# Performance work log

Hardware: AMD Instinct MI355X
Metric: run time of the kernel (lower is better)

The kernel has to match this reference:

```python
import jax, jax.numpy as jnp
import numpy as np

WINDOW_SIZES = (4, 8, 16, 32)


def setup_inputs() -> dict:
    key = jax.random.key(0)
    k1, k2 = jax.random.split(key)
    B, L, D = 128, 1024, 128
    sequence_emb = jax.random.normal(k1, (B, L, D), dtype=jnp.float32)
    mask = jax.random.randint(k2, (B, L), 0, 2, dtype=jnp.int32)
    return {"sequence_emb": sequence_emb, "mask": mask}


def reference(sequence_emb, mask):
    # sequence_emb: (B, L, D); mask: (B, L) int 0/1
    B, L, D = sequence_emb.shape
    m = mask.astype(sequence_emb.dtype)
    masked = sequence_emb * m[..., None]  # (B, L, D)
    # prefix sums with leading zero so window sum = cs[i+w] - cs[i]
    zero_v = jnp.zeros((B, 1, D), dtype=sequence_emb.dtype)
    cs = jnp.concatenate([zero_v, jnp.cumsum(masked, axis=1)], axis=1)  # (B, L+1, D)
    zero_m = jnp.zeros((B, 1), dtype=sequence_emb.dtype)
    cm = jnp.concatenate([zero_m, jnp.cumsum(m, axis=1)], axis=1)  # (B, L+1)
    outs = []
    for w in WINDOW_SIZES:
        if L < w:
            continue
        win_sum = cs[:, w:, :] - cs[:, :-w, :]          # (B, L-w+1, D)
        win_len = jnp.clip(cm[:, w:] - cm[:, :-w], 1.0)  # (B, L-w+1)
        outs.append(win_sum / win_len[..., None])
    return jnp.concatenate(outs, axis=1)  # (B, sum(L-w+1), D)
```

## Files before the change

kernel.cpp:

```cpp
#include <hip/hip_runtime.h>


namespace {
constexpr int kB    = 128;
constexpr int kL    = 1024;
constexpr int kD    = 128;
constexpr int kD4   = kD / 4;
constexpr int TILE  = 64;
constexpr int HALO  = 32;
constexpr int ROWS  = TILE + HALO;
constexpr int ROUT  = 4040;
constexpr int OFF4  = 0;
constexpr int OFF8  = 1021;
constexpr int OFF16 = 2038;
constexpr int OFF32 = 3047;
}

__device__ __forceinline__ void acc4(float4& a, const float4& x) {
    a.x += x.x; a.y += x.y; a.z += x.z; a.w += x.w;
}
__device__ __forceinline__ void slide4(float4& a, const float4& xin, const float4& xout) {
    a.x += xin.x - xout.x; a.y += xin.y - xout.y;
    a.z += xin.z - xout.z; a.w += xin.w - xout.w;
}
__device__ __forceinline__ float4 scale4(const float4& v, float s) {
    return make_float4(v.x * s, v.y * s, v.z * s, v.w * s);
}

__global__ __launch_bounds__(256)
void msse_kernel(const float* __restrict__ emb,
                 const int*   __restrict__ mask,
                 float*       __restrict__ out) {
    __shared__ float4 s_data[ROWS * kD4];
    __shared__ float  s_mask[ROWS];
    __shared__ float  s_inv[4][TILE];

    const int b  = blockIdx.y;
    const int i0 = blockIdx.x * TILE;
    const int t  = threadIdx.x;

    const float4* gsrc = reinterpret_cast<const float4*>(emb) + (size_t)b * kL * kD4;
    #pragma unroll
    for (int k = 0; k < (ROWS * kD4) / 256; ++k) {
        const int f    = t + k * 256;
        const int row  = f >> 5;
        const int grow = i0 + row;
        float4 v = make_float4(0.f, 0.f, 0.f, 0.f);
        float  m = 0.f;
        if (grow < kL) {
            m = (float)mask[b * kL + grow];
            v = gsrc[grow * kD4 + (f & 31)];
            v.x *= m; v.y *= m; v.z *= m; v.w *= m;
        }
        s_data[f] = v;
        if ((f & 31) == 0) s_mask[row] = m;
    }
    __syncthreads();

    if (t < TILE) {
        float c = 0.f, c4 = 0.f, c8 = 0.f, c16 = 0.f;
        #pragma unroll
        for (int j = 0; j < 32; ++j) {
            c += s_mask[t + j];
            if (j == 3)  c4  = c;
            if (j == 7)  c8  = c;
            if (j == 15) c16 = c;
        }
        s_inv[0][t] = 1.f / fmaxf(c4,  1.f);
        s_inv[1][t] = 1.f / fmaxf(c8,  1.f);
        s_inv[2][t] = 1.f / fmaxf(c16, 1.f);
        s_inv[3][t] = 1.f / fmaxf(c,   1.f);
    }
    __syncthreads();

    const int lane  = t & 31;
    const int strip = t >> 5;
    const int base  = strip * 8;

    const float4* col = s_data + lane;

    float4 s4, s8, s16, s32;
    {
        float4 a  = make_float4(0.f, 0.f, 0.f, 0.f);
        float4 t4 = a, t8 = a, t16 = a;
        #pragma unroll
        for (int j = 0; j < 32; ++j) {
            acc4(a, col[(base + j) * kD4]);
            if (j == 3)  t4  = a;
            if (j == 7)  t8  = a;
            if (j == 15) t16 = a;
        }
        s4 = t4; s8 = t8; s16 = t16; s32 = a;
    }

    float4* outb = reinterpret_cast<float4*>(out) + (size_t)b * ROUT * kD4 + lane;

    #pragma unroll
    for (int p = 0; p < 8; ++p) {
        const int il = base + p;
        const int i  = i0 + il;

        if (i <= kL - 4)  outb[(OFF4  + i) * kD4] = scale4(s4,  s_inv[0][il]);
        if (i <= kL - 8)  outb[(OFF8  + i) * kD4] = scale4(s8,  s_inv[1][il]);
        if (i <= kL - 16) outb[(OFF16 + i) * kD4] = scale4(s16, s_inv[2][il]);
        if (i <= kL - 32) outb[(OFF32 + i) * kD4] = scale4(s32, s_inv[3][il]);

        const float4 x0 = col[(il)      * kD4];
        const float4 xa = col[(il + 4)  * kD4];
        const float4 xb = col[(il + 8)  * kD4];
        const float4 xc = col[(il + 16) * kD4];
        const float4 xd = col[(il + 32) * kD4];
        slide4(s4,  xa, x0);
        slide4(s8,  xb, x0);
        slide4(s16, xc, x0);
        slide4(s32, xd, x0);
    }
}

extern "C" void kernel_launch(void* const* d_in, const int* in_sizes, int n_in,
                              void* d_out, int out_size, void* d_ws, size_t ws_size,
                              hipStream_t stream) {
    const float* emb  = (const float*)d_in[0];
    const int*   mask = (const int*)d_in[1];
    float*       out  = (float*)d_out;

    dim3 grid((kL + TILE - 1) / TILE, kB);
    dim3 block(256);
    msse_kernel<<<grid, block, 0, stream>>>(emb, mask, out);
}
```

Baseline: 315.8 us.

## Drop shared-memory staging, stream rows per wave with nontemporal stores and precomputed inverses

Replaces the LDS-tiled kernel with a per-wave strip design: each 64-lane wave owns 32 output positions of one batch row and reads embedding rows straight from global memory as float2, with each row re-read several times through the caches. Inverse window lengths move into a separate pre-kernel that writes float4 inverses to the workspace. Output stores become nontemporal. The aim is to remove LDS traffic and barriers and to raise occupancy. The cost is redundant global and L2 reads, a second kernel launch, and narrower 8-byte accesses.

```diff
diff --git a/kernel.cpp b/kernel.cpp
--- a/kernel.cpp
+++ b/kernel.cpp
@@ -2,90 +2,79 @@
 
 
 namespace {
-constexpr int kB    = 128;
-constexpr int kL    = 1024;
-constexpr int kD    = 128;
-constexpr int kD4   = kD / 4;
-constexpr int TILE  = 64;
-constexpr int HALO  = 32;
-constexpr int ROWS  = TILE + HALO;
-constexpr int ROUT  = 4040;
+constexpr int kB   = 128;
+constexpr int kL   = 1024;
+constexpr int kD   = 128;
+constexpr int kD2  = kD / 2;
+constexpr int ROUT = 4040;
 constexpr int OFF4  = 0;
 constexpr int OFF8  = 1021;
 constexpr int OFF16 = 2038;
 constexpr int OFF32 = 3047;
+constexpr int P    = 32;
+constexpr int STRIPS = kB * (kL / P);
 }
 
-__device__ __forceinline__ void acc4(float4& a, const float4& x) {
-    a.x += x.x; a.y += x.y; a.z += x.z; a.w += x.w;
+typedef float v2f __attribute__((ext_vector_type(2)));
+
+__device__ __forceinline__ void nt_store2(v2f* p, v2f v) {
+    __builtin_nontemporal_store(v, p);
 }
-__device__ __forceinline__ void slide4(float4& a, const float4& xin, const float4& xout) {
-    a.x += xin.x - xout.x; a.y += xin.y - xout.y;
-    a.z += xin.z - xout.z; a.w += xin.w - xout.w;
-}
-__device__ __forceinline__ float4 scale4(const float4& v, float s) {
-    return make_float4(v.x * s, v.y * s, v.z * s, v.w * s);
+
+__global__ __launch_bounds__(256)
+void inv_kernel(const int* __restrict__ mask, float4* __restrict__ invq) {
+    const int idx = blockIdx.x * 256 + threadIdx.x;
+    if (idx >= kB * kL) return;
+    const int i = idx & (kL - 1);
+    const int* mrow = mask + (idx - i);
+    float c = 0.f, c4 = 0.f, c8 = 0.f, c16 = 0.f;
+    #pragma unroll
+    for (int j = 0; j < 32; ++j) {
+        const int r = i + j;
+        const float m = (r < kL) ? (float)mrow[r] : 0.f;
+        c += m;
+        if (j == 3)  c4  = c;
+        if (j == 7)  c8  = c;
+        if (j == 15) c16 = c;
+    }
+    invq[idx] = make_float4(1.f / fmaxf(c4, 1.f), 1.f / fmaxf(c8, 1.f),
+                            1.f / fmaxf(c16, 1.f), 1.f / fmaxf(c, 1.f));
 }
 
 __global__ __launch_bounds__(256)
 void msse_kernel(const float* __restrict__ emb,
                  const int*   __restrict__ mask,
+                 const float4* __restrict__ invq,
                  float*       __restrict__ out) {
-    __shared__ float4 s_data[ROWS * kD4];
-    __shared__ float  s_mask[ROWS];
-    __shared__ float  s_inv[4][TILE];
+    const int wave  = threadIdx.x >> 6;
+    const int lane  = threadIdx.x & 63;
+    const int strip = blockIdx.x * 4 + wave;
+    const int b     = strip >> 5;
+    const int i0    = (strip & 31) * P;
 
-    const int b  = blockIdx.y;
-    const int i0 = blockIdx.x * TILE;
-    const int t  = threadIdx.x;
+    const v2f* __restrict__ e2 =
+        reinterpret_cast<const v2f*>(emb) + (size_t)b * kL * kD2 + lane;
+    const int* __restrict__ mrow = mask + b * kL;
+    const float4* __restrict__ ivq = invq + b * kL;
 
-    const float4* gsrc = reinterpret_cast<const float4*>(emb) + (size_t)b * kL * kD4;
-    #pragma unroll
-    for (int k = 0; k < (ROWS * kD4) / 256; ++k) {
-        const int f    = t + k * 256;
-        const int row  = f >> 5;
-        const int grow = i0 + row;
-        float4 v = make_float4(0.f, 0.f, 0.f, 0.f);
-        float  m = 0.f;
-        if (grow < kL) {
-            m = (float)mask[b * kL + grow];
-            v = gsrc[grow * kD4 + (f & 31)];
-            v.x *= m; v.y *= m; v.z *= m; v.w *= m;
+    auto loadrow = [&](int r) -> v2f {
+        v2f z; z.x = 0.f; z.y = 0.f;
+        if (r < kL) {
+            v2f v = e2[(size_t)r * kD2];
+            const float m = (float)mrow[r];
+            z.x = v.x * m; z.y = v.y * m;
         }
-        s_data[f] = v;
-        if ((f & 31) == 0) s_mask[row] = m;
-    }
-    __syncthreads();
+        return z;
+    };
 
-    if (t < TILE) {
-        float c = 0.f, c4 = 0.f, c8 = 0.f, c16 = 0.f;
+    v2f s4, s8, s16, s32;
+    {
+        v2f a; a.x = 0.f; a.y = 0.f;
+        v2f t4 = a, t8 = a, t16 = a;
         #pragma unroll
         for (int j = 0; j < 32; ++j) {
-            c += s_mask[t + j];
-            if (j == 3)  c4  = c;
-            if (j == 7)  c8  = c;
-            if (j == 15) c16 = c;
-        }
-        s_inv[0][t] = 1.f / fmaxf(c4,  1.f);
-        s_inv[1][t] = 1.f / fmaxf(c8,  1.f);
-        s_inv[2][t] = 1.f / fmaxf(c16, 1.f);
-        s_inv[3][t] = 1.f / fmaxf(c,   1.f);
-    }
-    __syncthreads();
-
-    const int lane  = t & 31;
-    const int strip = t >> 5;
-    const int base  = strip * 8;
-
-    const float4* col = s_data + lane;
-
-    float4 s4, s8, s16, s32;
-    {
-        float4 a  = make_float4(0.f, 0.f, 0.f, 0.f);
-        float4 t4 = a, t8 = a, t16 = a;
-        #pragma unroll
-        for (int j = 0; j < 32; ++j) {
-            acc4(a, col[(base + j) * kD4]);
+            const v2f x = loadrow(i0 + j);
+            a.x += x.x; a.y += x.y;
             if (j == 3)  t4  = a;
             if (j == 7)  t8  = a;
             if (j == 15) t16 = a;
@@ -93,27 +82,32 @@
         s4 = t4; s8 = t8; s16 = t16; s32 = a;
     }
 
-    float4* outb = reinterpret_cast<float4*>(out) + (size_t)b * ROUT * kD4 + lane;
+    v2f* ob = reinterpret_cast<v2f*>(out) + (size_t)b * ROUT * kD2 + lane;
 
-    #pragma unroll
-    for (int p = 0; p < 8; ++p) {
-        const int il = base + p;
-        const int i  = i0 + il;
+    #pragma unroll 4
+    for (int p = 0; p < P; ++p) {
+        const int i = i0 + p;
+        const float4 inv = ivq[i];
 
-        if (i <= kL - 4)  outb[(OFF4  + i) * kD4] = scale4(s4,  s_inv[0][il]);
-        if (i <= kL - 8)  outb[(OFF8  + i) * kD4] = scale4(s8,  s_inv[1][il]);
-        if (i <= kL - 16) outb[(OFF16 + i) * kD4] = scale4(s16, s_inv[2][il]);
-        if (i <= kL - 32) outb[(OFF32 + i) * kD4] = scale4(s32, s_inv[3][il]);
+        v2f o;
+        if (i <= kL - 4)  { o.x = s4.x  * inv.x; o.y = s4.y  * inv.x;
+                            nt_store2(ob + (size_t)(OFF4  + i) * kD2, o); }
+        if (i <= kL - 8)  { o.x = s8.x  * inv.y; o.y = s8.y  * inv.y;
+                            nt_store2(ob + (size_t)(OFF8  + i) * kD2, o); }
+        if (i <= kL - 16) { o.x = s16.x * inv.z; o.y = s16.y * inv.z;
+                            nt_store2(ob + (size_t)(OFF16 + i) * kD2, o); }
+        if (i <= kL - 32) { o.x = s32.x * inv.w; o.y = s32.y * inv.w;
+                            nt_store2(ob + (size_t)(OFF32 + i) * kD2, o); }
 
-        const float4 x0 = col[(il)      * kD4];
-        const float4 xa = col[(il + 4)  * kD4];
-        const float4 xb = col[(il + 8)  * kD4];
-        const float4 xc = col[(il + 16) * kD4];
-        const float4 xd = col[(il + 32) * kD4];
-        slide4(s4,  xa, x0);
-        slide4(s8,  xb, x0);
-        slide4(s16, xc, x0);
-        slide4(s32, xd, x0);
+        const v2f x0 = loadrow(i);
+        const v2f xa = loadrow(i + 4);
+        const v2f xb = loadrow(i + 8);
+        const v2f xc = loadrow(i + 16);
+        const v2f xd = loadrow(i + 32);
+        s4.x  += xa.x - x0.x;  s4.y  += xa.y - x0.y;
+        s8.x  += xb.x - x0.x;  s8.y  += xb.y - x0.y;
+        s16.x += xc.x - x0.x;  s16.y += xc.y - x0.y;
+        s32.x += xd.x - x0.x;  s32.y += xd.y - x0.y;
     }
 }
 
@@ -123,8 +117,8 @@
     const float* emb  = (const float*)d_in[0];
     const int*   mask = (const int*)d_in[1];
     float*       out  = (float*)d_out;
+    float4*      invq = (float4*)d_ws;
 
-    dim3 grid((kL + TILE - 1) / TILE, kB);
-    dim3 block(256);
-    msse_kernel<<<grid, block, 0, stream>>>(emb, mask, out);
+    inv_kernel<<<(kB * kL + 255) / 256, 256, 0, stream>>>(mask, invq);
+    msse_kernel<<<STRIPS / 4, 256, 0, stream>>>(emb, mask, invq, out);
 }
```

Measured after the change: 358.3 us. 13.5% more time.
